# Kernel optimization log

Hardware: AMD Instinct MI355X
Metric: run time of the kernel (lower is better)

The kernel has to match this reference:

```python
import jax, jax.numpy as jnp
import numpy as np


def setup_inputs() -> dict:
    key = jax.random.key(0)
    kq, kk, kv = jax.random.split(key, 3)
    B, S, H, D = 2, 2048, 32, 128
    q = jax.random.normal(kq, (B, S, H, D), dtype=jnp.float32)
    k = jax.random.normal(kk, (B, S, H, D), dtype=jnp.float32)
    v = jax.random.normal(kv, (B, S, H, D), dtype=jnp.float32)
    return {"q": q, "k": k, "v": v}


def _causal_attention(q, k, v):
    # q,k,v: [B, S, H, D] (flash-attn layout). Zigzag ring attention computes
    # exactly standard causal attention; zigzag only balances work across ranks.
    B, S, H, D = q.shape
    scale = 1.0 / jnp.sqrt(jnp.asarray(D, q.dtype))
    scores = jnp.einsum('bqhd,bkhd->bhqk', q, k) * scale  # [B,H,S,S]
    causal = jnp.tril(jnp.ones((S, S), dtype=bool))
    scores = jnp.where(causal, scores, jnp.finfo(scores.dtype).min)
    probs = jax.nn.softmax(scores, axis=-1)
    return jnp.einsum('bhqk,bkhd->bqhd', probs, v)  # [B,S,H,D]


def reference(q, k, v):
    out = _causal_attention(q, k, v)
    return jnp.sum(out)
```

## Files before the change

### kernel.cpp

```cpp
#include <hip/hip_runtime.h>
#include <hip/hip_bf16.h>
#include <stdint.h>

#define B_ 2
#define S_ 2048
#define H_ 32
#define D_ 128
#define R_ (B_*H_*S_)
#define PG 2048
#define QKU (2 * B_ * S_ * (H_/8))
#define VSU (B_ * S_)
#define CPB 40

typedef __bf16 bf16x8 __attribute__((ext_vector_type(8)));
typedef float  f32x16 __attribute__((ext_vector_type(16)));

#if __has_builtin(__builtin_amdgcn_exp2f)
#define EXP2F(x) __builtin_amdgcn_exp2f(x)
#else
#define EXP2F(x) exp2f(x)
#endif

#define AS1 __attribute__((address_space(1)))
#define AS3 __attribute__((address_space(3)))

__device__ __forceinline__ unsigned short f2bf(float f) {
  unsigned u = __float_as_uint(f);
  u += 0x7FFFu + ((u >> 16) & 1u);
  return (unsigned short)(u >> 16);
}

__global__ __launch_bounds__(256) void prep(
    const float* __restrict__ q, const float* __restrict__ k,
    const float* __restrict__ v,
    unsigned short* __restrict__ qb, unsigned short* __restrict__ kb,
    float* __restrict__ vsum, float* __restrict__ nd, float* __restrict__ out0) {
  const int bid = blockIdx.x;
  const int t = threadIdx.x;
  if (bid == 0 && t == 0) out0[0] = 0.f;

  #pragma unroll 4
  for (int g = 0; g < QKU / PG; ++g) {
    const int u = bid + g * PG;
    const int which = u >= (QKU / 2);
    const int i2 = which ? u - (QKU / 2) : u;
    const float* src = which ? k : q;
    unsigned short* dst = which ? kb : qb;
    const float sc = which ? 1.0f : 0.0883883476483184f * 1.4426950408889634f;
    const int b   = i2 / (S_ * 4);
    const int rem = i2 % (S_ * 4);
    const int s   = rem >> 2;
    const int h   = (rem & 3) * 8 + (t >> 5);
    const int lane32 = t & 31;
    const float4 v4 = *reinterpret_cast<const float4*>(
        src + (((size_t)b * S_ + s) * H_ + h) * D_ + lane32 * 4);
    ushort4 o;
    o.x = f2bf(v4.x * sc); o.y = f2bf(v4.y * sc);
    o.z = f2bf(v4.z * sc); o.w = f2bf(v4.w * sc);
    *reinterpret_cast<ushort4*>(
        dst + (((size_t)b * H_ + h) * S_ + s) * D_ + lane32 * 4) = o;
  }

  #pragma unroll
  for (int g = 0; g < VSU / PG; ++g) {
    const int u = bid + g * PG;
    const int b = u / S_, s = u % S_;
    const int h = t >> 3, i = t & 7;
    const float* p = v + (((size_t)b * S_ + s) * H_ + h) * D_ + i * 16;
    const float4 a0 = *reinterpret_cast<const float4*>(p + 0);
    const float4 a1 = *reinterpret_cast<const float4*>(p + 4);
    const float4 a2 = *reinterpret_cast<const float4*>(p + 8);
    const float4 a3 = *reinterpret_cast<const float4*>(p + 12);
    float sum = (a0.x+a0.y+a0.z+a0.w) + (a1.x+a1.y+a1.z+a1.w)
              + (a2.x+a2.y+a2.z+a2.w) + (a3.x+a3.y+a3.z+a3.w);
    sum += __shfl_xor(sum, 1);
    sum += __shfl_xor(sum, 2);
    sum += __shfl_xor(sum, 4);
    if (i == 0) vsum[((size_t)b * H_ + h) * S_ + s] = sum;
  }

  if (bid < 256) {
    float4* p = reinterpret_cast<float4*>(nd);
    p[(size_t)bid * 256 + t] = float4{0.f, 0.f, 0.f, 0.f};
  }
}

__global__ __launch_bounds__(256, 4) void attn_sum(
    const unsigned short* __restrict__ qg_, const unsigned short* __restrict__ kg_,
    const float* __restrict__ vsum, float* __restrict__ numb,
    float* __restrict__ denb) {
  __shared__ uint4 kbuf[4][512];
  __shared__ float vsbuf[4][64];

  const int id = blockIdx.x;
  const int y  = id >> 3;
  const int bh = (id & 7) + 8 * (y / CPB);
  const int c  = y % CPB;

  int qt, h, nch;
  if (c < 4)       { qt = c;                 h = 0;            nch = 1; }
  else if (c < 12) { qt = 4 + ((c - 4) >> 1);  h = (c - 4) & 1;  nch = 2; }
  else if (c < 24) { qt = 8 + (c - 12) / 3;    h = (c - 12) % 3; nch = 3; }
  else             { qt = 12 + ((c - 24) >> 2); h = (c - 24) & 3; nch = 4; }
  const int nkt  = 2 * qt + 2;
  const int bas_ = nkt / nch, rem = nkt % nch;
  const int kt0  = h * bas_ + (h < rem ? h : rem);
  const int kt1  = kt0 + bas_ + (h < rem ? 1 : 0);
  const int st0  = 2 * kt0, st1 = 2 * kt1;

  const int t  = threadIdx.x;
  const int w  = t >> 6;
  const int l  = t & 63;
  const int ln = l & 31, l5 = l >> 5;

  const size_t base = (size_t)bh * S_ * D_;
  const int qrow0 = qt * 128 + w * 32;
  const unsigned short* ksrc0 = kg_ + base;
  const float* vsrc0 = vsum + (size_t)bh * S_;

  bf16x8 qfrag[8];
  {
    const unsigned short* qp = qg_ + base + (size_t)(qrow0 + ln) * D_ + l5 * 8;
    #pragma unroll
    for (int kb8 = 0; kb8 < 8; ++kb8)
      qfrag[kb8] = *reinterpret_cast<const bf16x8*>(qp + kb8 * 16);
  }

  auto stage = [&](int st, int slot) {
    const unsigned short* ksrc = ksrc0 + (size_t)st * 32 * D_;
    #pragma unroll
    for (int j = 0; j < 2; ++j) {
      const int idx = (w * 2 + j) * 64 + l;
      const int r   = idx >> 4;
      const int p   = idx & 15;
      const int cc  = p ^ (r & 15);
      const unsigned short* src = ksrc + r * D_ + cc * 8;
      __builtin_amdgcn_global_load_lds(
          (const AS1 void*)src, (AS3 void*)(&kbuf[slot][idx & ~63]), 16, 0, 0);
    }
    __builtin_amdgcn_global_load_lds(
        (const AS1 void*)(vsrc0 + st * 32 + l), (AS3 void*)(&vsbuf[slot][0]), 4, 0, 0);
  };

  float num[16], den[16];
  #pragma unroll
  for (int r = 0; r < 16; ++r) { num[r] = 0.f; den[r] = 0.f; }

  stage(st0, st0 & 3);
  stage(st0 + 1, (st0 + 1) & 3);

  const int xr = ln & 15;
  for (int st = st0; st < st1; ++st) {
    if (st + 1 < st1) asm volatile("s_waitcnt vmcnt(3)" ::: "memory");
    else              asm volatile("s_waitcnt vmcnt(0)" ::: "memory");
    __builtin_amdgcn_s_barrier();
    if (st + 2 < st1) stage(st + 2, (st + 2) & 3);

    const int kbase = st * 32;
    if (kbase <= qrow0 + 31) {
      const int slot = st & 3;
      const uint4* rowb = &kbuf[slot][ln * 16];
      f32x16 sacc = {0.f,0.f,0.f,0.f,0.f,0.f,0.f,0.f,
                     0.f,0.f,0.f,0.f,0.f,0.f,0.f,0.f};
      __builtin_amdgcn_s_setprio(1);
      #pragma unroll
      for (int kb8 = 0; kb8 < 8; ++kb8) {
        const bf16x8 bf = *reinterpret_cast<const bf16x8*>(&rowb[(kb8 * 2 + l5) ^ xr]);
        sacc = __builtin_amdgcn_mfma_f32_32x32x16_bf16(qfrag[kb8], bf, sacc, 0, 0, 0);
      }
      __builtin_amdgcn_s_setprio(0);
      const float vsv = vsbuf[slot][ln];
      if (kbase + 31 <= qrow0) {
        #pragma unroll
        for (int r = 0; r < 16; ++r) {
          const float e = EXP2F(sacc[r]);
          den[r] += e;
          num[r] = fmaf(e, vsv, num[r]);
        }
      } else {
        const int kgc = kbase + ln;
        #pragma unroll
        for (int r = 0; r < 16; ++r) {
          const int qgr = qrow0 + (r & 3) + 8 * (r >> 2) + 4 * l5;
          const float e = (kgc <= qgr) ? EXP2F(sacc[r]) : 0.f;
          den[r] += e;
          num[r] = fmaf(e, vsv, num[r]);
        }
      }
    }
  }

  #pragma unroll
  for (int m = 1; m < 32; m <<= 1) {
    #pragma unroll
    for (int r = 0; r < 16; ++r) {
      num[r] += __shfl_xor(num[r], m);
      den[r] += __shfl_xor(den[r], m);
    }
  }
  if (ln == 0) {
    float* nrow = numb + (size_t)bh * S_;
    float* drow = denb + (size_t)bh * S_;
    #pragma unroll
    for (int r = 0; r < 16; ++r) {
      const int qgr = qrow0 + (r & 3) + 8 * (r >> 2) + 4 * l5;
      atomicAdd(&nrow[qgr], num[r]);
      atomicAdd(&drow[qgr], den[r]);
    }
  }
}

__global__ __launch_bounds__(256) void finalize(
    const float* __restrict__ numb, const float* __restrict__ denb,
    float* __restrict__ out) {
  const int i = blockIdx.x * 256 + threadIdx.x;
  float c = numb[i] / denb[i];
  #pragma unroll
  for (int m = 1; m < 64; m <<= 1) c += __shfl_xor(c, m);
  __shared__ float ps[4];
  if ((threadIdx.x & 63) == 0) ps[threadIdx.x >> 6] = c;
  __syncthreads();
  if (threadIdx.x == 0) atomicAdd(out, ps[0] + ps[1] + ps[2] + ps[3]);
}

extern "C" void kernel_launch(void* const* d_in, const int* in_sizes, int n_in,
                              void* d_out, int out_size, void* d_ws, size_t ws_size,
                              hipStream_t stream) {
  const float* q = (const float*)d_in[0];
  const float* k = (const float*)d_in[1];
  const float* v = (const float*)d_in[2];
  float* out = (float*)d_out;

  unsigned short* qb = (unsigned short*)d_ws;
  unsigned short* kb = qb + (size_t)R_ * D_;
  float* vsum = (float*)(kb + (size_t)R_ * D_);
  float* numb = vsum + R_;
  float* denb = numb + R_;

  hipLaunchKernelGGL(prep, dim3(PG), dim3(256), 0, stream,
                     q, k, v, qb, kb, vsum, numb, out);
  hipLaunchKernelGGL(attn_sum, dim3(64 * CPB), dim3(256), 0, stream,
                     qb, kb, vsum, numb, denb);
  hipLaunchKernelGGL(finalize, dim3(R_ / 256), dim3(256), 0, stream,
                     numb, denb, out);
}
```

Baseline: 120.5 us.

## Drop Q bf16 pre-conversion; convert Q in attention kernel, keep K in BSHD layout

The prep kernel no longer converts Q to a transposed bf16 buffer. The attention kernel now loads fp32 Q straight from the input and scales and rounds it into MFMA fragments in registers. K is still converted to bf16 but keeps its original [B,S,H,D] layout as a flat elementwise copy, and the K staging loads use a row stride of H*D. This removes a full Q write and read through the workspace and makes the K conversion fully coalesced, at the cost of redundant Q loads across the key-range chunks and strided 256-byte K row reads.

```diff
diff --git a/kernel.cpp b/kernel.cpp
--- a/kernel.cpp
+++ b/kernel.cpp
@@ -8,7 +8,6 @@
 #define D_ 128
 #define R_ (B_*H_*S_)
 #define PG 2048
-#define QKU (2 * B_ * S_ * (H_/8))
 #define VSU (B_ * S_)
 #define CPB 40
 
@@ -31,34 +30,23 @@
 }
 
 __global__ __launch_bounds__(256) void prep(
-    const float* __restrict__ q, const float* __restrict__ k,
-    const float* __restrict__ v,
-    unsigned short* __restrict__ qb, unsigned short* __restrict__ kb,
+    const float* __restrict__ k, const float* __restrict__ v,
+    unsigned short* __restrict__ kb,
     float* __restrict__ vsum, float* __restrict__ nd, float* __restrict__ out0) {
   const int bid = blockIdx.x;
   const int t = threadIdx.x;
   if (bid == 0 && t == 0) out0[0] = 0.f;
 
-  #pragma unroll 4
-  for (int g = 0; g < QKU / PG; ++g) {
-    const int u = bid + g * PG;
-    const int which = u >= (QKU / 2);
-    const int i2 = which ? u - (QKU / 2) : u;
-    const float* src = which ? k : q;
-    unsigned short* dst = which ? kb : qb;
-    const float sc = which ? 1.0f : 0.0883883476483184f * 1.4426950408889634f;
-    const int b   = i2 / (S_ * 4);
-    const int rem = i2 % (S_ * 4);
-    const int s   = rem >> 2;
-    const int h   = (rem & 3) * 8 + (t >> 5);
-    const int lane32 = t & 31;
-    const float4 v4 = *reinterpret_cast<const float4*>(
-        src + (((size_t)b * S_ + s) * H_ + h) * D_ + lane32 * 4);
-    ushort4 o;
-    o.x = f2bf(v4.x * sc); o.y = f2bf(v4.y * sc);
-    o.z = f2bf(v4.z * sc); o.w = f2bf(v4.w * sc);
-    *reinterpret_cast<ushort4*>(
-        dst + (((size_t)b * H_ + h) * S_ + s) * D_ + lane32 * 4) = o;
+  #pragma unroll
+  for (int g = 0; g < (R_ * D_ / 8) / (PG * 256); ++g) {
+    const size_t i = (size_t)g * (PG * 256) + bid * 256 + t;
+    const float4 a = *reinterpret_cast<const float4*>(k + i * 8);
+    const float4 b = *reinterpret_cast<const float4*>(k + i * 8 + 4);
+    ushort4 o0, o1;
+    o0.x = f2bf(a.x); o0.y = f2bf(a.y); o0.z = f2bf(a.z); o0.w = f2bf(a.w);
+    o1.x = f2bf(b.x); o1.y = f2bf(b.y); o1.z = f2bf(b.z); o1.w = f2bf(b.w);
+    *reinterpret_cast<ushort4*>(kb + i * 8)     = o0;
+    *reinterpret_cast<ushort4*>(kb + i * 8 + 4) = o1;
   }
 
   #pragma unroll
@@ -86,7 +74,7 @@
 }
 
 __global__ __launch_bounds__(256, 4) void attn_sum(
-    const unsigned short* __restrict__ qg_, const unsigned short* __restrict__ kg_,
+    const float* __restrict__ qf_, const unsigned short* __restrict__ kb_,
     const float* __restrict__ vsum, float* __restrict__ numb,
     float* __restrict__ denb) {
   __shared__ uint4 kbuf[4][512];
@@ -113,28 +101,36 @@
   const int l  = t & 63;
   const int ln = l & 31, l5 = l >> 5;
 
-  const size_t base = (size_t)bh * S_ * D_;
+  const int b0 = bh >> 5, h0 = bh & 31;
   const int qrow0 = qt * 128 + w * 32;
-  const unsigned short* ksrc0 = kg_ + base;
+  const unsigned short* ksrc0 = kb_ + ((size_t)b0 * S_ * H_ + h0) * D_;
   const float* vsrc0 = vsum + (size_t)bh * S_;
 
+  const float sc = 0.0883883476483184f * 1.4426950408889634f;
   bf16x8 qfrag[8];
   {
-    const unsigned short* qp = qg_ + base + (size_t)(qrow0 + ln) * D_ + l5 * 8;
-    #pragma unroll
-    for (int kb8 = 0; kb8 < 8; ++kb8)
-      qfrag[kb8] = *reinterpret_cast<const bf16x8*>(qp + kb8 * 16);
+    const float* qp = qf_ + (((size_t)b0 * S_ + qrow0 + ln) * H_ + h0) * D_ + l5 * 8;
+    #pragma unroll
+    for (int kb8 = 0; kb8 < 8; ++kb8) {
+      const float4 a = *reinterpret_cast<const float4*>(qp + kb8 * 16);
+      const float4 b = *reinterpret_cast<const float4*>(qp + kb8 * 16 + 4);
+      union { unsigned short u[8]; bf16x8 v; } uu;
+      uu.u[0] = f2bf(a.x * sc); uu.u[1] = f2bf(a.y * sc);
+      uu.u[2] = f2bf(a.z * sc); uu.u[3] = f2bf(a.w * sc);
+      uu.u[4] = f2bf(b.x * sc); uu.u[5] = f2bf(b.y * sc);
+      uu.u[6] = f2bf(b.z * sc); uu.u[7] = f2bf(b.w * sc);
+      qfrag[kb8] = uu.v;
+    }
   }
 
   auto stage = [&](int st, int slot) {
-    const unsigned short* ksrc = ksrc0 + (size_t)st * 32 * D_;
     #pragma unroll
     for (int j = 0; j < 2; ++j) {
       const int idx = (w * 2 + j) * 64 + l;
       const int r   = idx >> 4;
       const int p   = idx & 15;
       const int cc  = p ^ (r & 15);
-      const unsigned short* src = ksrc + r * D_ + cc * 8;
+      const unsigned short* src = ksrc0 + (size_t)(st * 32 + r) * (H_ * D_) + cc * 8;
       __builtin_amdgcn_global_load_lds(
           (const AS1 void*)src, (AS3 void*)(&kbuf[slot][idx & ~63]), 16, 0, 0);
     }
@@ -231,16 +227,15 @@
   const float* v = (const float*)d_in[2];
   float* out = (float*)d_out;
 
-  unsigned short* qb = (unsigned short*)d_ws;
-  unsigned short* kb = qb + (size_t)R_ * D_;
+  unsigned short* kb = (unsigned short*)d_ws;
   float* vsum = (float*)(kb + (size_t)R_ * D_);
   float* numb = vsum + R_;
   float* denb = numb + R_;
 
   hipLaunchKernelGGL(prep, dim3(PG), dim3(256), 0, stream,
-                     q, k, v, qb, kb, vsum, numb, out);
+                     k, v, kb, vsum, numb, out);
   hipLaunchKernelGGL(attn_sum, dim3(64 * CPB), dim3(256), 0, stream,
-                     qb, kb, vsum, numb, denb);
+                     q, kb, vsum, numb, denb);
   hipLaunchKernelGGL(finalize, dim3(R_ / 256), dim3(256), 0, stream,
                      numb, denb, out);
 }
```

Result: faster. 111.5 us (-7.4%).
